# Kernel optimization log

Hardware: AMD Instinct MI355X
Metric: run time of the kernel (lower is better)

Reference implementation:

```python
import jax, jax.numpy as jnp
import numpy as np

TAU = 2.0   # membrane time constant
V_TH = 0.5  # firing threshold

@jax.custom_vjp
def spike_fn(v):
    return jnp.where(v > 0, 1.0, 0.0)

def _spike_fwd(v):
    return spike_fn(v), v

def _spike_bwd(v, g):
    # atan surrogate gradient (alpha=2): d s / d v = 1 / (1 + (pi*v)^2)
    sg = 1.0 / (1.0 + (jnp.pi * v) ** 2)
    return (g * sg,)

spike_fn.defvjp(_spike_fwd, _spike_bwd)


def setup_inputs() -> dict:
    key = jax.random.key(0)
    # [batch, neurons, time] -- time on axis 2, matching moveaxis(x, 2, 0)
    x = jax.random.normal(key, (32, 16384, 100), dtype=jnp.float32)
    return {"x": x}


def reference(x):
    x_seq = jnp.moveaxis(x, 2, 0)  # [T, B, N]
    decay = 1.0 - 1.0 / TAU

    def scan_fn(v, x_t):
        v = v * decay + x_t            # leaky integrate
        s = spike_fn(v - V_TH)         # fire
        v = v - s * V_TH               # soft reset
        return v, s

    v_init = jnp.zeros_like(x_seq[0])
    _, spikes = jax.lax.scan(scan_fn, v_init, x_seq)
    return jnp.moveaxis(spikes, 0, 2)  # [B, N, T]
```

## Files before the change

kernel.cpp:

```cpp
#include <hip/hip_runtime.h>


#define T_STEPS 100
#define T_VEC   25
#define ROWS    64
#define RSTRIDE 100
#define DECAY   0.5f
#define VTH     0.5f

typedef float vfloat4 __attribute__((ext_vector_type(4)));

__device__ __forceinline__ int eswz(int r) { return (r ^ (r >> 3)) & 7; }
__device__ __forceinline__ int slot(int r, int c) {
    int cs = (c < 24) ? (c ^ eswz(r)) : 24;
    return r * RSTRIDE + cs * 4;
}

__global__ __launch_bounds__(64) void lif_kernel(const float* __restrict__ x,
                                                 float* __restrict__ out,
                                                 int n_rows) {
    __shared__ float tile[ROWS * RSTRIDE];
    __shared__ unsigned int bits[ROWS * 4];

    const int lane = threadIdx.x;
    const long long row0 = (long long)blockIdx.x * ROWS;
    const long long gf0 = row0 * T_VEC;
    const long long total_f4 = (long long)n_rows * T_VEC;

    const vfloat4* __restrict__ xb = reinterpret_cast<const vfloat4*>(x);

    {
        vfloat4 st[13];
        #pragma unroll
        for (int k = 0; k < 13; ++k) {
            long long g = gf0 + k * 64 + lane;
            vfloat4 z = {0.0f, 0.0f, 0.0f, 0.0f};
            st[k] = (g < total_f4) ? xb[g] : z;
        }
        #pragma unroll
        for (int k = 0; k < 13; ++k) {
            int f = k * 64 + lane;
            int r = f / T_VEC, c = f % T_VEC;
            *reinterpret_cast<vfloat4*>(&tile[slot(r, c)]) = st[k];
        }
    }
    {
        vfloat4 st[12];
        #pragma unroll
        for (int k = 0; k < 12; ++k) {
            long long g = gf0 + (13 + k) * 64 + lane;
            vfloat4 z = {0.0f, 0.0f, 0.0f, 0.0f};
            st[k] = (g < total_f4) ? xb[g] : z;
        }
        #pragma unroll
        for (int k = 0; k < 12; ++k) {
            int f = (13 + k) * 64 + lane;
            int r = f / T_VEC, c = f % T_VEC;
            *reinterpret_cast<vfloat4*>(&tile[slot(r, c)]) = st[k];
        }
    }

    unsigned int pk0 = 0, pk1 = 0, pk2 = 0, pk3 = 0;
    {
        float v = 0.0f;
        #pragma unroll
        for (int c = 0; c < T_VEC; ++c) {
            vfloat4 xs = *reinterpret_cast<const vfloat4*>(&tile[slot(lane, c)]);
            #pragma unroll
            for (int k = 0; k < 4; ++k) {
                v = v * DECAY + xs[k];
                bool sb = (v - VTH > 0.0f);
                v -= sb ? VTH : 0.0f;
                unsigned int bit = sb ? 1u : 0u;
                const int b = c * 4 + k;
                if (b < 32)      pk0 |= bit << b;
                else if (b < 64) pk1 |= bit << (b - 32);
                else if (b < 96) pk2 |= bit << (b - 64);
                else             pk3 |= bit << (b - 96);
            }
        }
    }

    {
        uint4 w; w.x = pk0; w.y = pk1; w.z = pk2; w.w = pk3;
        reinterpret_cast<uint4*>(bits)[lane] = w;
    }
    __syncthreads();

    vfloat4* __restrict__ ob = reinterpret_cast<vfloat4*>(out);
    #pragma unroll
    for (int i = 0; i < T_VEC; ++i) {
        int f = i * 64 + lane;
        long long g = gf0 + f;
        if (g < total_f4) {
            int r  = f / T_VEC;
            int c4 = f % T_VEC;
            unsigned int word = bits[r * 4 + (c4 >> 3)];
            int shift = (c4 & 7) * 4;
            unsigned int nib = (word >> shift) & 0xFu;
            vfloat4 s;
            s.x = (nib & 1u) ? 1.0f : 0.0f;
            s.y = (nib & 2u) ? 1.0f : 0.0f;
            s.z = (nib & 4u) ? 1.0f : 0.0f;
            s.w = (nib & 8u) ? 1.0f : 0.0f;
            ob[g] = s;
        }
    }
}

extern "C" void kernel_launch(void* const* d_in, const int* in_sizes, int n_in,
                              void* d_out, int out_size, void* d_ws, size_t ws_size,
                              hipStream_t stream) {
    const float* x = (const float*)d_in[0];
    float* out = (float*)d_out;

    int n_rows = in_sizes[0] / T_STEPS;
    int grid = (n_rows + ROWS - 1) / ROWS;

    lif_kernel<<<grid, ROWS, 0, stream>>>(x, out, n_rows);
}
```

Baseline: 89.56 us.

## Split LDS staging into two halves to overlap second load with first compute

The time dimension is split into two chunks of 12 and 13 float4s. The kernel stages the first chunk in a smaller LDS tile, issues the global loads for the second chunk into registers, and runs the scan over the first chunk while those loads are in flight. It then reuses the same tile for the second chunk. This roughly halves LDS use, adds a min-blocks launch bound to raise occupancy, and switches indexing to 32-bit ints, at the cost of extra barriers and higher register pressure.

```diff
diff --git a/kernel.cpp b/kernel.cpp
--- a/kernel.cpp
+++ b/kernel.cpp
@@ -4,80 +4,95 @@
 #define T_STEPS 100
 #define T_VEC   25
 #define ROWS    64
-#define RSTRIDE 100
+#define CA      12
+#define CB      13
+#define LSTRIDE 13
 #define DECAY   0.5f
 #define VTH     0.5f
 
 typedef float vfloat4 __attribute__((ext_vector_type(4)));
 
-__device__ __forceinline__ int eswz(int r) { return (r ^ (r >> 3)) & 7; }
-__device__ __forceinline__ int slot(int r, int c) {
-    int cs = (c < 24) ? (c ^ eswz(r)) : 24;
-    return r * RSTRIDE + cs * 4;
-}
-
-__global__ __launch_bounds__(64) void lif_kernel(const float* __restrict__ x,
-                                                 float* __restrict__ out,
-                                                 int n_rows) {
-    __shared__ float tile[ROWS * RSTRIDE];
+__global__ __launch_bounds__(64, 3) void lif_kernel(const float* __restrict__ x,
+                                                    float* __restrict__ out,
+                                                    int n_rows) {
+    __shared__ vfloat4 tile[ROWS * LSTRIDE];
     __shared__ unsigned int bits[ROWS * 4];
 
     const int lane = threadIdx.x;
-    const long long row0 = (long long)blockIdx.x * ROWS;
-    const long long gf0 = row0 * T_VEC;
-    const long long total_f4 = (long long)n_rows * T_VEC;
+    const int row0 = blockIdx.x * ROWS;
+    const int gf0 = row0 * T_VEC;
+    const int total_f4 = n_rows * T_VEC;
 
     const vfloat4* __restrict__ xb = reinterpret_cast<const vfloat4*>(x);
+    const vfloat4 vzero = {0.0f, 0.0f, 0.0f, 0.0f};
 
     {
-        vfloat4 st[13];
+        vfloat4 st[CA];
         #pragma unroll
-        for (int k = 0; k < 13; ++k) {
-            long long g = gf0 + k * 64 + lane;
-            vfloat4 z = {0.0f, 0.0f, 0.0f, 0.0f};
-            st[k] = (g < total_f4) ? xb[g] : z;
+        for (int k = 0; k < CA; ++k) {
+            int f = k * 64 + lane;
+            int r = f / CA, c = f % CA;
+            int g = gf0 + r * T_VEC + c;
+            st[k] = (g < total_f4) ? xb[g] : vzero;
         }
         #pragma unroll
-        for (int k = 0; k < 13; ++k) {
+        for (int k = 0; k < CA; ++k) {
             int f = k * 64 + lane;
-            int r = f / T_VEC, c = f % T_VEC;
-            *reinterpret_cast<vfloat4*>(&tile[slot(r, c)]) = st[k];
+            int r = f / CA, c = f % CA;
+            tile[r * LSTRIDE + c] = st[k];
         }
     }
-    {
-        vfloat4 st[12];
+    __syncthreads();
+
+    vfloat4 sb[CB];
+    #pragma unroll
+    for (int k = 0; k < CB; ++k) {
+        int f = k * 64 + lane;
+        int r = f / CB, c = f % CB;
+        int g = gf0 + r * T_VEC + CA + c;
+        sb[k] = (g < total_f4) ? xb[g] : vzero;
+    }
+    __builtin_amdgcn_sched_barrier(0);
+
+    unsigned int pk0 = 0, pk1 = 0, pk2 = 0, pk3 = 0;
+    float v = 0.0f;
+    #pragma unroll
+    for (int c = 0; c < CA; ++c) {
+        vfloat4 xs = tile[lane * LSTRIDE + c];
         #pragma unroll
-        for (int k = 0; k < 12; ++k) {
-            long long g = gf0 + (13 + k) * 64 + lane;
-            vfloat4 z = {0.0f, 0.0f, 0.0f, 0.0f};
-            st[k] = (g < total_f4) ? xb[g] : z;
-        }
-        #pragma unroll
-        for (int k = 0; k < 12; ++k) {
-            int f = (13 + k) * 64 + lane;
-            int r = f / T_VEC, c = f % T_VEC;
-            *reinterpret_cast<vfloat4*>(&tile[slot(r, c)]) = st[k];
+        for (int k = 0; k < 4; ++k) {
+            v = v * DECAY + xs[k];
+            bool s = (v - VTH > 0.0f);
+            v -= s ? VTH : 0.0f;
+            unsigned int bit = s ? 1u : 0u;
+            const int b = c * 4 + k;
+            if (b < 32) pk0 |= bit << b;
+            else        pk1 |= bit << (b - 32);
         }
     }
+    __syncthreads();
 
-    unsigned int pk0 = 0, pk1 = 0, pk2 = 0, pk3 = 0;
-    {
-        float v = 0.0f;
+    #pragma unroll
+    for (int k = 0; k < CB; ++k) {
+        int f = k * 64 + lane;
+        int r = f / CB, c = f % CB;
+        tile[r * LSTRIDE + c] = sb[k];
+    }
+    __syncthreads();
+
+    #pragma unroll
+    for (int c = 0; c < CB; ++c) {
+        vfloat4 xs = tile[lane * LSTRIDE + c];
         #pragma unroll
-        for (int c = 0; c < T_VEC; ++c) {
-            vfloat4 xs = *reinterpret_cast<const vfloat4*>(&tile[slot(lane, c)]);
-            #pragma unroll
-            for (int k = 0; k < 4; ++k) {
-                v = v * DECAY + xs[k];
-                bool sb = (v - VTH > 0.0f);
-                v -= sb ? VTH : 0.0f;
-                unsigned int bit = sb ? 1u : 0u;
-                const int b = c * 4 + k;
-                if (b < 32)      pk0 |= bit << b;
-                else if (b < 64) pk1 |= bit << (b - 32);
-                else if (b < 96) pk2 |= bit << (b - 64);
-                else             pk3 |= bit << (b - 96);
-            }
+        for (int k = 0; k < 4; ++k) {
+            v = v * DECAY + xs[k];
+            bool s = (v - VTH > 0.0f);
+            v -= s ? VTH : 0.0f;
+            unsigned int bit = s ? 1u : 0u;
+            const int b = 48 + c * 4 + k;
+            if (b < 64)      pk1 |= bit << (b - 32);
+            else if (b < 96) pk2 |= bit << (b - 64);
+            else             pk3 |= bit << (b - 96);
         }
     }
 
@@ -91,7 +106,7 @@
     #pragma unroll
     for (int i = 0; i < T_VEC; ++i) {
         int f = i * 64 + lane;
-        long long g = gf0 + f;
+        int g = gf0 + f;
         if (g < total_f4) {
             int r  = f / T_VEC;
             int c4 = f % T_VEC;
```

Measured after the change: 91.28 us. Within noise of the previous version (+1.9%).

## Persistent grid-stride LIF kernel with register prefetch of next tile

Applied to the files above, without the earlier changes.

Replaces the one-shot kernel (one 64-row tile per block) with a fixed grid of 3072 blocks. Each block loops over 32-row tiles and prefetches the next tile into registers while it computes and stores the current one. The aim is to overlap global loads with the scan and the output writes, and to cut block launch overhead. In exchange only half the wave does the recurrence, the LDS swizzle is dropped so row-strided LDS reads may bank-conflict, and the smaller grid lowers the number of waves resident per CU on a bandwidth-bound kernel.

```diff
diff --git a/kernel.cpp b/kernel.cpp
--- a/kernel.cpp
+++ b/kernel.cpp
@@ -3,108 +3,115 @@
 
 #define T_STEPS 100
 #define T_VEC   25
-#define ROWS    64
-#define RSTRIDE 100
+#define TROWS   32
+#define TF4     (TROWS * T_VEC)
+#define NLD     13
+#define GRID    3072
 #define DECAY   0.5f
 #define VTH     0.5f
 
 typedef float vfloat4 __attribute__((ext_vector_type(4)));
 
-__device__ __forceinline__ int eswz(int r) { return (r ^ (r >> 3)) & 7; }
-__device__ __forceinline__ int slot(int r, int c) {
-    int cs = (c < 24) ? (c ^ eswz(r)) : 24;
-    return r * RSTRIDE + cs * 4;
-}
-
-__global__ __launch_bounds__(64) void lif_kernel(const float* __restrict__ x,
-                                                 float* __restrict__ out,
-                                                 int n_rows) {
-    __shared__ float tile[ROWS * RSTRIDE];
-    __shared__ unsigned int bits[ROWS * 4];
+__global__ __launch_bounds__(64) void lif_pipe(const float* __restrict__ x,
+                                               float* __restrict__ out,
+                                               int n_rows) {
+    __shared__ vfloat4 tile[TF4];
+    __shared__ uint4   bitsbuf[TROWS];
 
     const int lane = threadIdx.x;
-    const long long row0 = (long long)blockIdx.x * ROWS;
-    const long long gf0 = row0 * T_VEC;
-    const long long total_f4 = (long long)n_rows * T_VEC;
+    const int ntiles = (n_rows + TROWS - 1) / TROWS;
+    const int total_f4 = n_rows * T_VEC;
+    const vfloat4* __restrict__ xb = reinterpret_cast<const vfloat4*>(x);
+    vfloat4* __restrict__ ob = reinterpret_cast<vfloat4*>(out);
+    const vfloat4 vz = {0.0f, 0.0f, 0.0f, 0.0f};
 
-    const vfloat4* __restrict__ xb = reinterpret_cast<const vfloat4*>(x);
+    int t = blockIdx.x;
+    if (t >= ntiles) return;
+
+    vfloat4 st[NLD];
 
     {
-        vfloat4 st[13];
+        int base = t * TF4;
         #pragma unroll
-        for (int k = 0; k < 13; ++k) {
-            long long g = gf0 + k * 64 + lane;
-            vfloat4 z = {0.0f, 0.0f, 0.0f, 0.0f};
-            st[k] = (g < total_f4) ? xb[g] : z;
+        for (int k = 0; k < NLD; ++k) {
+            int f = k * 64 + lane;
+            st[k] = (f < TF4 && base + f < total_f4) ? xb[base + f] : vz;
         }
         #pragma unroll
-        for (int k = 0; k < 13; ++k) {
+        for (int k = 0; k < NLD; ++k) {
             int f = k * 64 + lane;
-            int r = f / T_VEC, c = f % T_VEC;
-            *reinterpret_cast<vfloat4*>(&tile[slot(r, c)]) = st[k];
+            if (f < TF4) tile[f] = st[k];
         }
     }
-    {
-        vfloat4 st[12];
-        #pragma unroll
-        for (int k = 0; k < 12; ++k) {
-            long long g = gf0 + (13 + k) * 64 + lane;
-            vfloat4 z = {0.0f, 0.0f, 0.0f, 0.0f};
-            st[k] = (g < total_f4) ? xb[g] : z;
-        }
-        #pragma unroll
-        for (int k = 0; k < 12; ++k) {
-            int f = (13 + k) * 64 + lane;
-            int r = f / T_VEC, c = f % T_VEC;
-            *reinterpret_cast<vfloat4*>(&tile[slot(r, c)]) = st[k];
-        }
-    }
+    __builtin_amdgcn_sched_barrier(0);
 
-    unsigned int pk0 = 0, pk1 = 0, pk2 = 0, pk3 = 0;
-    {
-        float v = 0.0f;
-        #pragma unroll
-        for (int c = 0; c < T_VEC; ++c) {
-            vfloat4 xs = *reinterpret_cast<const vfloat4*>(&tile[slot(lane, c)]);
+    for (; t < ntiles; t += GRID) {
+        const int tn = t + GRID;
+
+        if (tn < ntiles) {
+            int base = tn * TF4;
             #pragma unroll
-            for (int k = 0; k < 4; ++k) {
-                v = v * DECAY + xs[k];
-                bool sb = (v - VTH > 0.0f);
-                v -= sb ? VTH : 0.0f;
-                unsigned int bit = sb ? 1u : 0u;
-                const int b = c * 4 + k;
-                if (b < 32)      pk0 |= bit << b;
-                else if (b < 64) pk1 |= bit << (b - 32);
-                else if (b < 96) pk2 |= bit << (b - 64);
-                else             pk3 |= bit << (b - 96);
+            for (int k = 0; k < NLD; ++k) {
+                int f = k * 64 + lane;
+                st[k] = (f < TF4 && base + f < total_f4) ? xb[base + f] : vz;
             }
         }
-    }
+        __builtin_amdgcn_sched_barrier(0);
 
-    {
-        uint4 w; w.x = pk0; w.y = pk1; w.z = pk2; w.w = pk3;
-        reinterpret_cast<uint4*>(bits)[lane] = w;
-    }
-    __syncthreads();
+        if (lane < TROWS) {
+            unsigned int pk0 = 0, pk1 = 0, pk2 = 0, pk3 = 0;
+            float v = 0.0f;
+            #pragma unroll
+            for (int c = 0; c < T_VEC; ++c) {
+                vfloat4 xs = tile[lane * T_VEC + c];
+                #pragma unroll
+                for (int k = 0; k < 4; ++k) {
+                    v = v * DECAY + xs[k];
+                    bool s = (v - VTH > 0.0f);
+                    v -= s ? VTH : 0.0f;
+                    unsigned int bit = s ? 1u : 0u;
+                    const int b = c * 4 + k;
+                    if      (b < 32) pk0 |= bit << b;
+                    else if (b < 64) pk1 |= bit << (b - 32);
+                    else if (b < 96) pk2 |= bit << (b - 64);
+                    else             pk3 |= bit << (b - 96);
+                }
+            }
+            uint4 w; w.x = pk0; w.y = pk1; w.z = pk2; w.w = pk3;
+            bitsbuf[lane] = w;
+        }
+        __builtin_amdgcn_sched_barrier(0);
 
-    vfloat4* __restrict__ ob = reinterpret_cast<vfloat4*>(out);
-    #pragma unroll
-    for (int i = 0; i < T_VEC; ++i) {
-        int f = i * 64 + lane;
-        long long g = gf0 + f;
-        if (g < total_f4) {
-            int r  = f / T_VEC;
-            int c4 = f % T_VEC;
-            unsigned int word = bits[r * 4 + (c4 >> 3)];
-            int shift = (c4 & 7) * 4;
-            unsigned int nib = (word >> shift) & 0xFu;
-            vfloat4 s;
-            s.x = (nib & 1u) ? 1.0f : 0.0f;
-            s.y = (nib & 2u) ? 1.0f : 0.0f;
-            s.z = (nib & 4u) ? 1.0f : 0.0f;
-            s.w = (nib & 8u) ? 1.0f : 0.0f;
-            ob[g] = s;
+        {
+            int base = t * TF4;
+            #pragma unroll
+            for (int i = 0; i < NLD; ++i) {
+                int lf = i * 64 + lane;
+                if (lf < TF4 && base + lf < total_f4) {
+                    int r  = lf / T_VEC;
+                    int c4 = lf % T_VEC;
+                    unsigned int word =
+                        reinterpret_cast<const unsigned int*>(bitsbuf)[r * 4 + (c4 >> 3)];
+                    unsigned int nib = (word >> ((c4 & 7) * 4)) & 0xFu;
+                    vfloat4 s;
+                    s.x = (nib & 1u) ? 1.0f : 0.0f;
+                    s.y = (nib & 2u) ? 1.0f : 0.0f;
+                    s.z = (nib & 4u) ? 1.0f : 0.0f;
+                    s.w = (nib & 8u) ? 1.0f : 0.0f;
+                    ob[base + lf] = s;
+                }
+            }
         }
+        __builtin_amdgcn_sched_barrier(0);
+
+        if (tn < ntiles) {
+            #pragma unroll
+            for (int k = 0; k < NLD; ++k) {
+                int f = k * 64 + lane;
+                if (f < TF4) tile[f] = st[k];
+            }
+        }
+        __builtin_amdgcn_sched_barrier(0);
     }
 }
 
@@ -115,7 +122,8 @@
     float* out = (float*)d_out;
 
     int n_rows = in_sizes[0] / T_STEPS;
-    int grid = (n_rows + ROWS - 1) / ROWS;
+    int ntiles = (n_rows + TROWS - 1) / TROWS;
+    int grid = (ntiles < GRID) ? ntiles : GRID;
 
-    lif_kernel<<<grid, ROWS, 0, stream>>>(x, out, n_rows);
+    lif_pipe<<<grid, 64, 0, stream>>>(x, out, n_rows);
 }
```

Result: slower. 96.11 us (+7.3%).
